# Kernel tuning notes

Measured on AMD Instinct MI355X. Metric: run time of the kernel, lower is better.

## Reference

```python
import jax, jax.numpy as jnp
import numpy as np

N_NODES = 100000


def gcn_conv(x, src, dst, W, b):
    # x: [N, F_in]; src/dst include self-loops; symmetric degree normalization (PyG GCNConv)
    n = x.shape[0]
    xw = x @ W  # [N, F_out]
    ones = jnp.ones(dst.shape[0], dtype=xw.dtype)
    deg = jax.ops.segment_sum(ones, dst, num_segments=n)  # in-degree incl. self-loop
    dinv = jnp.where(deg > 0, jax.lax.rsqrt(deg), 0.0)
    norm = dinv[src] * dinv[dst]  # [E]
    msg = xw[src] * norm[:, None]  # gather + per-edge scale
    out = jax.ops.segment_sum(msg, dst, num_segments=n)  # scatter-add aggregation
    return out + b


def setup_inputs() -> dict:
    key = jax.random.key(0)
    ks = jax.random.split(key, 6)
    F_in = 512
    E = 3200000
    x = jax.random.normal(ks[0], (N_NODES, F_in), dtype=jnp.float32)
    edge_index = jax.random.randint(ks[1], (2, E), 0, N_NODES, dtype=jnp.int64)
    W1 = jax.random.normal(ks[2], (F_in, 16), dtype=jnp.float32) * (1.0 / np.sqrt(F_in))
    b1 = jnp.zeros((16,), dtype=jnp.float32)
    W2 = jax.random.normal(ks[3], (16, 16), dtype=jnp.float32) * 0.25
    b2 = jnp.zeros((16,), dtype=jnp.float32)
    fc_w = jax.random.normal(ks[4], (16, 1), dtype=jnp.float32) * 0.25
    fc_b = jnp.zeros((1,), dtype=jnp.float32)
    return {"x": x, "edge_index": edge_index, "W1": W1, "b1": b1,
            "W2": W2, "b2": b2, "fc_w": fc_w, "fc_b": fc_b}


def reference(x, edge_index, W1, b1, W2, b2, fc_w, fc_b):
    n = x.shape[0]
    loop = jnp.arange(n, dtype=edge_index.dtype)
    src = jnp.concatenate([edge_index[0], loop])  # add self-loops
    dst = jnp.concatenate([edge_index[1], loop])
    h = jax.nn.relu(gcn_conv(x, src, dst, W1, b1))
    h = jax.nn.relu(gcn_conv(h, src, dst, W2, b2))
    g = jnp.mean(h, axis=0, keepdims=True)  # global_mean_pool, single graph -> [1, 16]
    return g @ fc_w + fc_b  # [1, 1]
```

## Files before the change

kernel.cpp:

```cpp
#include <hip/hip_runtime.h>
#include <hip/hip_fp16.h>
#include <stdint.h>

#define F_IN 512
#define F_OUT 16
#define CB_SHIFT 8
#define CB_W 256
#define PER 6250
#define SORT_CAP 6400

typedef __attribute__((ext_vector_type(8))) short bf16x8;
typedef __attribute__((ext_vector_type(4))) float f32x4;

__device__ inline float4 f4_shfl_xor(float4 v, int mask) {
    float4 r;
    r.x = __shfl_xor(v.x, mask);
    r.y = __shfl_xor(v.y, mask);
    r.z = __shfl_xor(v.z, mask);
    r.w = __shfl_xor(v.w, mask);
    return r;
}

__device__ inline short f2bf(float f) {
    unsigned u = __float_as_uint(f);
    unsigned r = (u + 0x7FFFu + ((u >> 16) & 1u)) >> 16;
    return (short)(unsigned short)r;
}

__device__ inline float4 ld_h4(const __half* __restrict__ xw, int s, int q) {
    const __half2* p = (const __half2*)(xw + ((size_t)s << 4)) + (q << 1);
    float2 f0 = __half22float2(p[0]);
    float2 f1 = __half22float2(p[1]);
    return make_float4(f0.x, f0.y, f1.x, f1.y);
}

__global__ __launch_bounds__(256) void k_chist(const int* __restrict__ ei, int E, int K1, int B,
                                               int* __restrict__ cntT) {
    __shared__ int h[512];
    int t = threadIdx.x;
    for (int i = t; i < K1; i += 256) h[i] = 0;
    __syncthreads();
    int e0 = blockIdx.x * PER, e1 = min(E, e0 + PER);
    for (int e = e0 + t; e < e1; e += 256)
        atomicAdd(&h[ei[(size_t)E + e] >> CB_SHIFT], 1);
    __syncthreads();
    for (int i = t; i < K1; i += 256) cntT[(size_t)i * B + blockIdx.x] = h[i];
}

__global__ __launch_bounds__(512) void k_btot(const int* __restrict__ cntT, int B, int K1,
                                              int* __restrict__ bucketBase, int* __restrict__ bucketCnt) {
    __shared__ int sm[512];
    int k = threadIdx.x;
    int tot = 0;
    if (k < K1) {
        const int4* row = (const int4*)(cntT + (size_t)k * B);
        for (int b = 0; b < B / 4; b++) {
            int4 v = row[b];
            tot += v.x + v.y + v.z + v.w;
        }
    }
    sm[k] = tot;
    __syncthreads();
    for (int off = 1; off < 512; off <<= 1) {
        int add = (k >= off) ? sm[k - off] : 0;
        __syncthreads();
        sm[k] += add;
        __syncthreads();
    }
    if (k < K1) { bucketBase[k] = sm[k] - tot; bucketCnt[k] = tot; }
}

__global__ __launch_bounds__(512) void k_bbase(const int* __restrict__ cntT, int B,
                                               const int* __restrict__ bucketBase,
                                               int* __restrict__ baseT) {
    __shared__ int sm[512];
    int k = blockIdx.x, t = threadIdx.x;
    int v = (t < B) ? cntT[(size_t)k * B + t] : 0;
    sm[t] = v;
    __syncthreads();
    for (int off = 1; off < 512; off <<= 1) {
        int add = (t >= off) ? sm[t - off] : 0;
        __syncthreads();
        sm[t] += add;
        __syncthreads();
    }
    if (t < B) baseT[(size_t)k * B + t] = bucketBase[k] + sm[t] - v;
}

__global__ __launch_bounds__(512) void k_csort(const int* __restrict__ ei, int E, int K1, int B,
                                               const int* __restrict__ baseT, unsigned* __restrict__ part) {
    __shared__ unsigned sorted[SORT_CAP];
    __shared__ int h[512], lb[512], cur[512], gb[512];
    int t = threadIdx.x;
    int e0 = blockIdx.x * PER, e1 = min(E, e0 + PER);
    h[t] = 0;
    __syncthreads();
    for (int e = e0 + t; e < e1; e += 512)
        atomicAdd(&h[ei[(size_t)E + e] >> CB_SHIFT], 1);
    __syncthreads();
    int v = h[t];
    lb[t] = v;
    __syncthreads();
    for (int off = 1; off < 512; off <<= 1) {
        int add = (t >= off) ? lb[t - off] : 0;
        __syncthreads();
        lb[t] += add;
        __syncthreads();
    }
    int excl = lb[t] - v;
    __syncthreads();
    lb[t] = excl;
    cur[t] = excl;
    if (t < K1) gb[t] = baseT[(size_t)t * B + blockIdx.x];
    __syncthreads();
    for (int e = e0 + t; e < e1; e += 512) {
        int s = ei[e];
        int d = ei[(size_t)E + e];
        int pos = atomicAdd(&cur[d >> CB_SHIFT], 1);
        sorted[pos] = ((unsigned)s << CB_SHIFT) | (unsigned)(d & (CB_W - 1));
    }
    __syncthreads();
    int g16 = t >> 4, ln = t & 15;
    for (int k = g16; k < K1; k += 32) {
        int s0 = lb[k];
        int s1 = cur[k];
        int g  = gb[k];
        for (int i = s0 + ln; i < s1; i += 16)
            part[(size_t)g + (i - s0)] = sorted[i];
    }
}

__global__ __launch_bounds__(512) void k_prep2(const unsigned* __restrict__ part,
                                               const int* __restrict__ bucketBase, const int* __restrict__ bucketCnt,
                                               int* __restrict__ hist, float* __restrict__ dinv,
                                               int* __restrict__ offsets, int* __restrict__ csr, int N) {
    __shared__ int fh[CB_W], fb[CB_W], cur[CB_W];
    int k = blockIdx.x, t = threadIdx.x;
    int base = bucketBase[k], cnt = bucketCnt[k];
    int d0 = k << CB_SHIFT;
    if (t < CB_W) fh[t] = 0;
    __syncthreads();
    for (int i = t; i < cnt; i += 512)
        atomicAdd(&fh[part[(size_t)base + i] & (CB_W - 1)], 1);
    __syncthreads();
    int v = 0;
    if (t < CB_W) { v = fh[t]; fb[t] = v; }
    __syncthreads();
    for (int off = 1; off < CB_W; off <<= 1) {
        int add = (t >= off && t < CB_W) ? fb[t - off] : 0;
        __syncthreads();
        if (t < CB_W) fb[t] += add;
        __syncthreads();
    }
    if (t < CB_W) {
        int excl = fb[t] - v;
        int n = d0 + t;
        if (n < N) {
            offsets[n] = base + excl;
            hist[n] = v;
            dinv[n] = rsqrtf((float)(v + 1));
        }
        cur[t] = excl;
    }
    __syncthreads();
    for (int i = t; i < cnt; i += 512) {
        unsigned e = part[(size_t)base + i];
        int pos = atomicAdd(&cur[e & (CB_W - 1)], 1);
        csr[(size_t)base + pos] = (int)(e >> CB_SHIFT);
    }
}

__global__ __launch_bounds__(256, 4) void k_gemm1(const float* __restrict__ x, const float* __restrict__ W1,
                                                  const float* __restrict__ dinv, __half* __restrict__ xw1p, int N) {
    int lane = threadIdx.x & 63;
    int wv   = blockIdx.x * 4 + (threadIdx.x >> 6);
    int nw   = gridDim.x * 4;
    int r16  = lane & 15;
    int kg   = lane >> 4;

    bf16x8 bfrag[16];
#pragma unroll
    for (int s = 0; s < 16; s++) {
        bf16x8 f;
#pragma unroll
        for (int i = 0; i < 8; i++)
            f[i] = f2bf(W1[(s * 32 + kg * 8 + i) * 16 + r16]);
        bfrag[s] = f;
    }

    int ntiles = (N + 15) >> 4;
    int npairs = (ntiles + 1) >> 1;
    for (int pair = wv; pair < npairs; pair += nw) {
        int tile0 = pair * 2;
        int tile1 = tile0 + 1;
        int row0 = (tile0 << 4) + r16;
        int row1 = (tile1 << 4) + r16;
        const float* xr0 = x + (size_t)min(row0, N - 1) * F_IN + kg * 8;
        const float* xr1 = x + (size_t)min(row1, N - 1) * F_IN + kg * 8;
        bool t1ok = (tile1 < ntiles);
        f32x4 acc0 = {0.f, 0.f, 0.f, 0.f};
        f32x4 acc1 = {0.f, 0.f, 0.f, 0.f};
#pragma unroll
        for (int s = 0; s < 16; s++) {
            float4 xa0 = *(const float4*)(xr0 + s * 32);
            float4 xb0 = *(const float4*)(xr0 + s * 32 + 4);
            float4 xa1 = *(const float4*)(xr1 + s * 32);
            float4 xb1 = *(const float4*)(xr1 + s * 32 + 4);
            bf16x8 af0, af1;
            af0[0] = f2bf(xa0.x); af0[1] = f2bf(xa0.y); af0[2] = f2bf(xa0.z); af0[3] = f2bf(xa0.w);
            af0[4] = f2bf(xb0.x); af0[5] = f2bf(xb0.y); af0[6] = f2bf(xb0.z); af0[7] = f2bf(xb0.w);
            af1[0] = f2bf(xa1.x); af1[1] = f2bf(xa1.y); af1[2] = f2bf(xa1.z); af1[3] = f2bf(xa1.w);
            af1[4] = f2bf(xb1.x); af1[5] = f2bf(xb1.y); af1[6] = f2bf(xb1.z); af1[7] = f2bf(xb1.w);
            acc0 = __builtin_amdgcn_mfma_f32_16x16x32_bf16(af0, bfrag[s], acc0, 0, 0, 0);
            acc1 = __builtin_amdgcn_mfma_f32_16x16x32_bf16(af1, bfrag[s], acc1, 0, 0, 0);
        }
#pragma unroll
        for (int j = 0; j < 4; j++) {
            int r0 = (tile0 << 4) + kg * 4 + j;
            if (r0 < N) {
                float dn = dinv[r0];
                xw1p[((size_t)r0 << 4) + r16] = __float2half_rn(dn * acc0[j]);
            }
        }
        if (t1ok) {
#pragma unroll
            for (int j = 0; j < 4; j++) {
                int r1 = (tile1 << 4) + kg * 4 + j;
                if (r1 < N) {
                    float dn = dinv[r1];
                    xw1p[((size_t)r1 << 4) + r16] = __float2half_rn(dn * acc1[j]);
                }
            }
        }
    }
}

__global__ __launch_bounds__(256) void k_agg1(const __half* __restrict__ xw, const int* __restrict__ offsets,
                                              const int* __restrict__ hist, const float* __restrict__ dinv,
                                              const int* __restrict__ csr, const float* __restrict__ b1,
                                              const float* __restrict__ W2, __half* __restrict__ xw2p, int N) {
    __shared__ float W2s[256];
    if (threadIdx.x < 256) W2s[threadIdx.x] = W2[threadIdx.x];
    __syncthreads();

    int lane = threadIdx.x & 63;
    int wave = threadIdx.x >> 6;
    int grp  = lane >> 4;
    int sub  = lane & 15;
    int eo   = sub >> 2;
    int q    = sub & 3;
    int node = blockIdx.x * 16 + wave * 4 + grp;
    if (node >= N) return;

    int start = offsets[node], cnt = hist[node];
    float dn = dinv[node];
    float4 a0 = make_float4(0.f,0.f,0.f,0.f), a1 = a0, a2 = a0, a3 = a0;
    int i = 0;
    for (; i + 32 <= cnt; i += 32) {
        int s0 = csr[start + i + eo];
        int s1 = csr[start + i + 4 + eo];
        int s2 = csr[start + i + 8 + eo];
        int s3 = csr[start + i + 12 + eo];
        int s4 = csr[start + i + 16 + eo];
        int s5 = csr[start + i + 20 + eo];
        int s6 = csr[start + i + 24 + eo];
        int s7 = csr[start + i + 28 + eo];
        float4 v0 = ld_h4(xw, s0, q);
        float4 v1 = ld_h4(xw, s1, q);
        float4 v2 = ld_h4(xw, s2, q);
        float4 v3 = ld_h4(xw, s3, q);
        float4 v4 = ld_h4(xw, s4, q);
        float4 v5 = ld_h4(xw, s5, q);
        float4 v6 = ld_h4(xw, s6, q);
        float4 v7 = ld_h4(xw, s7, q);
        a0.x+=v0.x; a0.y+=v0.y; a0.z+=v0.z; a0.w+=v0.w;
        a1.x+=v1.x; a1.y+=v1.y; a1.z+=v1.z; a1.w+=v1.w;
        a2.x+=v2.x; a2.y+=v2.y; a2.z+=v2.z; a2.w+=v2.w;
        a3.x+=v3.x; a3.y+=v3.y; a3.z+=v3.z; a3.w+=v3.w;
        a0.x+=v4.x; a0.y+=v4.y; a0.z+=v4.z; a0.w+=v4.w;
        a1.x+=v5.x; a1.y+=v5.y; a1.z+=v5.z; a1.w+=v5.w;
        a2.x+=v6.x; a2.y+=v6.y; a2.z+=v6.z; a2.w+=v6.w;
        a3.x+=v7.x; a3.y+=v7.y; a3.z+=v7.z; a3.w+=v7.w;
    }
    for (; i + 16 <= cnt; i += 16) {
        int s0 = csr[start + i + eo];
        int s1 = csr[start + i + 4 + eo];
        int s2 = csr[start + i + 8 + eo];
        int s3 = csr[start + i + 12 + eo];
        float4 v0 = ld_h4(xw, s0, q);
        float4 v1 = ld_h4(xw, s1, q);
        float4 v2 = ld_h4(xw, s2, q);
        float4 v3 = ld_h4(xw, s3, q);
        a0.x+=v0.x; a0.y+=v0.y; a0.z+=v0.z; a0.w+=v0.w;
        a1.x+=v1.x; a1.y+=v1.y; a1.z+=v1.z; a1.w+=v1.w;
        a2.x+=v2.x; a2.y+=v2.y; a2.z+=v2.z; a2.w+=v2.w;
        a3.x+=v3.x; a3.y+=v3.y; a3.z+=v3.z; a3.w+=v3.w;
    }
    for (; i + 8 <= cnt; i += 8) {
        int s0 = csr[start + i + eo];
        int s1 = csr[start + i + 4 + eo];
        float4 v0 = ld_h4(xw, s0, q);
        float4 v1 = ld_h4(xw, s1, q);
        a0.x+=v0.x; a0.y+=v0.y; a0.z+=v0.z; a0.w+=v0.w;
        a1.x+=v1.x; a1.y+=v1.y; a1.z+=v1.z; a1.w+=v1.w;
    }
    for (; i < cnt; i += 4) {
        if (i + eo < cnt) {
            int s0 = csr[start + i + eo];
            float4 v0 = ld_h4(xw, s0, q);
            a0.x+=v0.x; a0.y+=v0.y; a0.z+=v0.z; a0.w+=v0.w;
        }
    }
    float4 acc;
    acc.x = a0.x+a1.x+a2.x+a3.x;
    acc.y = a0.y+a1.y+a2.y+a3.y;
    acc.z = a0.z+a1.z+a2.z+a3.z;
    acc.w = a0.w+a1.w+a2.w+a3.w;
    { float4 u = f4_shfl_xor(acc, 4); acc.x+=u.x; acc.y+=u.y; acc.z+=u.z; acc.w+=u.w; }
    { float4 u = f4_shfl_xor(acc, 8); acc.x+=u.x; acc.y+=u.y; acc.z+=u.z; acc.w+=u.w; }

    float4 sv = ld_h4(xw, node, q);
    float4 bq = ((const float4*)b1)[q];
    float4 h;
    h.x = fmaxf(dn * (acc.x + sv.x) + bq.x, 0.f);
    h.y = fmaxf(dn * (acc.y + sv.y) + bq.y, 0.f);
    h.z = fmaxf(dn * (acc.z + sv.z) + bq.z, 0.f);
    h.w = fmaxf(dn * (acc.w + sv.w) + bq.w, 0.f);

    float o = 0.f;
#pragma unroll
    for (int a = 0; a < 4; a++) {
        int src = (grp << 4) + a;
        float h0 = __shfl(h.x, src);
        float h1 = __shfl(h.y, src);
        float h2 = __shfl(h.z, src);
        float h3 = __shfl(h.w, src);
        o += h0 * W2s[(a*4+0)*16 + sub] + h1 * W2s[(a*4+1)*16 + sub]
           + h2 * W2s[(a*4+2)*16 + sub] + h3 * W2s[(a*4+3)*16 + sub];
    }
    xw2p[((size_t)node << 4) + sub] = __float2half_rn(dn * o);
}

__global__ __launch_bounds__(256) void k_agg2(const __half* __restrict__ xw, const int* __restrict__ offsets,
                                              const int* __restrict__ hist, const float* __restrict__ dinv,
                                              const int* __restrict__ csr, const float* __restrict__ b2,
                                              float* __restrict__ partials, int N) {
    int lane = threadIdx.x & 63;
    int wave = threadIdx.x >> 6;
    int grp  = lane >> 4;
    int sub  = lane & 15;
    int eo   = sub >> 2;
    int q    = sub & 3;
    int node = blockIdx.x * 16 + wave * 4 + grp;

    float4 m = make_float4(0.f, 0.f, 0.f, 0.f);
    if (node < N) {
        int start = offsets[node], cnt = hist[node];
        float dn = dinv[node];
        float4 a0 = make_float4(0.f,0.f,0.f,0.f), a1 = a0, a2 = a0, a3 = a0;
        int i = 0;
        for (; i + 32 <= cnt; i += 32) {
            int s0 = csr[start + i + eo];
            int s1 = csr[start + i + 4 + eo];
            int s2 = csr[start + i + 8 + eo];
            int s3 = csr[start + i + 12 + eo];
            int s4 = csr[start + i + 16 + eo];
            int s5 = csr[start + i + 20 + eo];
            int s6 = csr[start + i + 24 + eo];
            int s7 = csr[start + i + 28 + eo];
            float4 v0 = ld_h4(xw, s0, q);
            float4 v1 = ld_h4(xw, s1, q);
            float4 v2 = ld_h4(xw, s2, q);
            float4 v3 = ld_h4(xw, s3, q);
            float4 v4 = ld_h4(xw, s4, q);
            float4 v5 = ld_h4(xw, s5, q);
            float4 v6 = ld_h4(xw, s6, q);
            float4 v7 = ld_h4(xw, s7, q);
            a0.x+=v0.x; a0.y+=v0.y; a0.z+=v0.z; a0.w+=v0.w;
            a1.x+=v1.x; a1.y+=v1.y; a1.z+=v1.z; a1.w+=v1.w;
            a2.x+=v2.x; a2.y+=v2.y; a2.z+=v2.z; a2.w+=v2.w;
            a3.x+=v3.x; a3.y+=v3.y; a3.z+=v3.z; a3.w+=v3.w;
            a0.x+=v4.x; a0.y+=v4.y; a0.z+=v4.z; a0.w+=v4.w;
            a1.x+=v5.x; a1.y+=v5.y; a1.z+=v5.z; a1.w+=v5.w;
            a2.x+=v6.x; a2.y+=v6.y; a2.z+=v6.z; a2.w+=v6.w;
            a3.x+=v7.x; a3.y+=v7.y; a3.z+=v7.z; a3.w+=v7.w;
        }
        for (; i + 16 <= cnt; i += 16) {
            int s0 = csr[start + i + eo];
            int s1 = csr[start + i + 4 + eo];
            int s2 = csr[start + i + 8 + eo];
            int s3 = csr[start + i + 12 + eo];
            float4 v0 = ld_h4(xw, s0, q);
            float4 v1 = ld_h4(xw, s1, q);
            float4 v2 = ld_h4(xw, s2, q);
            float4 v3 = ld_h4(xw, s3, q);
            a0.x+=v0.x; a0.y+=v0.y; a0.z+=v0.z; a0.w+=v0.w;
            a1.x+=v1.x; a1.y+=v1.y; a1.z+=v1.z; a1.w+=v1.w;
            a2.x+=v2.x; a2.y+=v2.y; a2.z+=v2.z; a2.w+=v2.w;
            a3.x+=v3.x; a3.y+=v3.y; a3.z+=v3.z; a3.w+=v3.w;
        }
        for (; i + 8 <= cnt; i += 8) {
            int s0 = csr[start + i + eo];
            int s1 = csr[start + i + 4 + eo];
            float4 v0 = ld_h4(xw, s0, q);
            float4 v1 = ld_h4(xw, s1, q);
            a0.x+=v0.x; a0.y+=v0.y; a0.z+=v0.z; a0.w+=v0.w;
            a1.x+=v1.x; a1.y+=v1.y; a1.z+=v1.z; a1.w+=v1.w;
        }
        for (; i < cnt; i += 4) {
            if (i + eo < cnt) {
                int s0 = csr[start + i + eo];
                float4 v0 = ld_h4(xw, s0, q);
                a0.x+=v0.x; a0.y+=v0.y; a0.z+=v0.z; a0.w+=v0.w;
            }
        }
        float4 acc;
        acc.x = a0.x+a1.x+a2.x+a3.x;
        acc.y = a0.y+a1.y+a2.y+a3.y;
        acc.z = a0.z+a1.z+a2.z+a3.z;
        acc.w = a0.w+a1.w+a2.w+a3.w;
        { float4 u = f4_shfl_xor(acc, 4); acc.x+=u.x; acc.y+=u.y; acc.z+=u.z; acc.w+=u.w; }
        { float4 u = f4_shfl_xor(acc, 8); acc.x+=u.x; acc.y+=u.y; acc.z+=u.z; acc.w+=u.w; }
        float4 sv = ld_h4(xw, node, q);
        float4 bq = ((const float4*)b2)[q];
        if (eo == 0) {
            m.x = fmaxf(dn * (acc.x + sv.x) + bq.x, 0.f);
            m.y = fmaxf(dn * (acc.y + sv.y) + bq.y, 0.f);
            m.z = fmaxf(dn * (acc.z + sv.z) + bq.z, 0.f);
            m.w = fmaxf(dn * (acc.w + sv.w) + bq.w, 0.f);
        }
    }
    { float4 u = f4_shfl_xor(m, 16); m.x+=u.x; m.y+=u.y; m.z+=u.z; m.w+=u.w; }
    { float4 u = f4_shfl_xor(m, 32); m.x+=u.x; m.y+=u.y; m.z+=u.z; m.w+=u.w; }
    __shared__ float smf[4][16];
    if (lane < 4) {
        smf[wave][q*4+0] = m.x;
        smf[wave][q*4+1] = m.y;
        smf[wave][q*4+2] = m.z;
        smf[wave][q*4+3] = m.w;
    }
    __syncthreads();
    if (threadIdx.x < 16) {
        float s = smf[0][threadIdx.x] + smf[1][threadIdx.x] + smf[2][threadIdx.x] + smf[3][threadIdx.x];
        partials[(size_t)blockIdx.x * 16 + threadIdx.x] = s;
    }
}

__global__ void k_final(const float* __restrict__ partials, int NB, const float* __restrict__ fc_w,
                        const float* __restrict__ fc_b, float* __restrict__ out, float invN) {
    __shared__ float sm[64][16];
    int t = threadIdx.x;
    int g = t >> 4, j = t & 15;
    float s = 0.0f;
    for (int bk = g; bk < NB; bk += 64) s += partials[(size_t)bk * 16 + j];
    sm[g][j] = s;
    __syncthreads();
    for (int str = 32; str > 0; str >>= 1) {
        if (g < str) sm[g][j] += sm[g + str][j];
        __syncthreads();
    }
    if (t == 0) {
        float acc = fc_b[0];
#pragma unroll
        for (int jj = 0; jj < 16; jj++) acc += sm[0][jj] * invN * fc_w[jj];
        out[0] = acc;
    }
}

extern "C" void kernel_launch(void* const* d_in, const int* in_sizes, int n_in,
                              void* d_out, int out_size, void* d_ws, size_t ws_size,
                              hipStream_t stream) {
    const float* x   = (const float*)d_in[0];
    const int*   ei  = (const int*)d_in[1];
    const float* W1  = (const float*)d_in[2];
    const float* b1  = (const float*)d_in[3];
    const float* W2  = (const float*)d_in[4];
    const float* b2  = (const float*)d_in[5];
    const float* fcw = (const float*)d_in[6];
    const float* fcb = (const float*)d_in[7];
    float* out = (float*)d_out;

    int N = in_sizes[0] / F_IN;
    int E = in_sizes[1] / 2;
    int K1 = (N + CB_W - 1) >> CB_SHIFT;
    int B1 = (E + PER - 1) / PER;

    char* p = (char*)d_ws;
    auto alloc = [&](size_t bytes) {
        void* r = (void*)p;
        p += (bytes + 255) & ~(size_t)255;
        return r;
    };
    int*   cntT       = (int*)alloc((size_t)K1 * B1 * 4);
    int*   baseT      = (int*)alloc((size_t)K1 * B1 * 4);
    int*   bucketBase = (int*)alloc((size_t)K1 * 4);
    int*   bucketCnt  = (int*)alloc((size_t)K1 * 4);
    int*   hist       = (int*)alloc((size_t)N * 4);
    int*   offsets    = (int*)alloc((size_t)N * 4);
    float* dinv       = (float*)alloc((size_t)N * 4);
    int*   csr        = (int*)alloc((size_t)E * 4);
    unsigned* part    = (unsigned*)alloc((size_t)E * 4);
    __half* xw1p      = (__half*)alloc((size_t)N * F_OUT * 2);
    __half* xw2p      = (__half*)alloc((size_t)N * F_OUT * 2);
    int NB_NODE = (N + 15) / 16;
    float* partials = (float*)alloc((size_t)NB_NODE * 16 * 4);

    k_chist<<<B1, 256, 0, stream>>>(ei, E, K1, B1, cntT);
    k_btot<<<1, 512, 0, stream>>>(cntT, B1, K1, bucketBase, bucketCnt);
    k_bbase<<<K1, 512, 0, stream>>>(cntT, B1, bucketBase, baseT);
    k_csort<<<B1, 512, 0, stream>>>(ei, E, K1, B1, baseT, part);
    k_prep2<<<K1, 512, 0, stream>>>(part, bucketBase, bucketCnt, hist, dinv, offsets, csr, N);

    k_gemm1<<<782, 256, 0, stream>>>(x, W1, dinv, xw1p, N);
    k_agg1<<<NB_NODE, 256, 0, stream>>>(xw1p, offsets, hist, dinv, csr, b1, W2, xw2p, N);
    k_agg2<<<NB_NODE, 256, 0, stream>>>(xw2p, offsets, hist, dinv, csr, b2, partials, N);
    k_final<<<1, 1024, 0, stream>>>(partials, NB_NODE, fcw, fcb, out, 1.0f / (float)N);
}
```

Measured before the change: 213.9 us.

## Split GEMM1 across CSR-build kernels to overlap compute with sorting

The dense x@W1 GEMM is cut into three row-pair ranges, each run by extra blocks appended to the histogram, bucket-sort and CSR-finalize kernels, so the memory-bound x read overlaps the edge-sorting phases. Because dinv is not known until the last phase, the GEMM now writes unscaled fp16 results and a new k_scale pass multiplies by dinv afterwards. The csort kernel also reuses the per-block histogram from cntT instead of recomputing it. The cost is an extra read-modify-write pass over xw1, plus hand-tuned split ratios and grid sizes that may leave the work unevenly balanced.

After: 250.3 us. 17.0% more time.

```diff
diff --git a/kernel.cpp b/kernel.cpp
--- a/kernel.cpp
+++ b/kernel.cpp
@@ -34,147 +34,10 @@
     return make_float4(f0.x, f0.y, f1.x, f1.y);
 }
 
-__global__ __launch_bounds__(256) void k_chist(const int* __restrict__ ei, int E, int K1, int B,
-                                               int* __restrict__ cntT) {
-    __shared__ int h[512];
-    int t = threadIdx.x;
-    for (int i = t; i < K1; i += 256) h[i] = 0;
-    __syncthreads();
-    int e0 = blockIdx.x * PER, e1 = min(E, e0 + PER);
-    for (int e = e0 + t; e < e1; e += 256)
-        atomicAdd(&h[ei[(size_t)E + e] >> CB_SHIFT], 1);
-    __syncthreads();
-    for (int i = t; i < K1; i += 256) cntT[(size_t)i * B + blockIdx.x] = h[i];
-}
-
-__global__ __launch_bounds__(512) void k_btot(const int* __restrict__ cntT, int B, int K1,
-                                              int* __restrict__ bucketBase, int* __restrict__ bucketCnt) {
-    __shared__ int sm[512];
-    int k = threadIdx.x;
-    int tot = 0;
-    if (k < K1) {
-        const int4* row = (const int4*)(cntT + (size_t)k * B);
-        for (int b = 0; b < B / 4; b++) {
-            int4 v = row[b];
-            tot += v.x + v.y + v.z + v.w;
-        }
-    }
-    sm[k] = tot;
-    __syncthreads();
-    for (int off = 1; off < 512; off <<= 1) {
-        int add = (k >= off) ? sm[k - off] : 0;
-        __syncthreads();
-        sm[k] += add;
-        __syncthreads();
-    }
-    if (k < K1) { bucketBase[k] = sm[k] - tot; bucketCnt[k] = tot; }
-}
-
-__global__ __launch_bounds__(512) void k_bbase(const int* __restrict__ cntT, int B,
-                                               const int* __restrict__ bucketBase,
-                                               int* __restrict__ baseT) {
-    __shared__ int sm[512];
-    int k = blockIdx.x, t = threadIdx.x;
-    int v = (t < B) ? cntT[(size_t)k * B + t] : 0;
-    sm[t] = v;
-    __syncthreads();
-    for (int off = 1; off < 512; off <<= 1) {
-        int add = (t >= off) ? sm[t - off] : 0;
-        __syncthreads();
-        sm[t] += add;
-        __syncthreads();
-    }
-    if (t < B) baseT[(size_t)k * B + t] = bucketBase[k] + sm[t] - v;
-}
-
-__global__ __launch_bounds__(512) void k_csort(const int* __restrict__ ei, int E, int K1, int B,
-                                               const int* __restrict__ baseT, unsigned* __restrict__ part) {
-    __shared__ unsigned sorted[SORT_CAP];
-    __shared__ int h[512], lb[512], cur[512], gb[512];
-    int t = threadIdx.x;
-    int e0 = blockIdx.x * PER, e1 = min(E, e0 + PER);
-    h[t] = 0;
-    __syncthreads();
-    for (int e = e0 + t; e < e1; e += 512)
-        atomicAdd(&h[ei[(size_t)E + e] >> CB_SHIFT], 1);
-    __syncthreads();
-    int v = h[t];
-    lb[t] = v;
-    __syncthreads();
-    for (int off = 1; off < 512; off <<= 1) {
-        int add = (t >= off) ? lb[t - off] : 0;
-        __syncthreads();
-        lb[t] += add;
-        __syncthreads();
-    }
-    int excl = lb[t] - v;
-    __syncthreads();
-    lb[t] = excl;
-    cur[t] = excl;
-    if (t < K1) gb[t] = baseT[(size_t)t * B + blockIdx.x];
-    __syncthreads();
-    for (int e = e0 + t; e < e1; e += 512) {
-        int s = ei[e];
-        int d = ei[(size_t)E + e];
-        int pos = atomicAdd(&cur[d >> CB_SHIFT], 1);
-        sorted[pos] = ((unsigned)s << CB_SHIFT) | (unsigned)(d & (CB_W - 1));
-    }
-    __syncthreads();
-    int g16 = t >> 4, ln = t & 15;
-    for (int k = g16; k < K1; k += 32) {
-        int s0 = lb[k];
-        int s1 = cur[k];
-        int g  = gb[k];
-        for (int i = s0 + ln; i < s1; i += 16)
-            part[(size_t)g + (i - s0)] = sorted[i];
-    }
-}
-
-__global__ __launch_bounds__(512) void k_prep2(const unsigned* __restrict__ part,
-                                               const int* __restrict__ bucketBase, const int* __restrict__ bucketCnt,
-                                               int* __restrict__ hist, float* __restrict__ dinv,
-                                               int* __restrict__ offsets, int* __restrict__ csr, int N) {
-    __shared__ int fh[CB_W], fb[CB_W], cur[CB_W];
-    int k = blockIdx.x, t = threadIdx.x;
-    int base = bucketBase[k], cnt = bucketCnt[k];
-    int d0 = k << CB_SHIFT;
-    if (t < CB_W) fh[t] = 0;
-    __syncthreads();
-    for (int i = t; i < cnt; i += 512)
-        atomicAdd(&fh[part[(size_t)base + i] & (CB_W - 1)], 1);
-    __syncthreads();
-    int v = 0;
-    if (t < CB_W) { v = fh[t]; fb[t] = v; }
-    __syncthreads();
-    for (int off = 1; off < CB_W; off <<= 1) {
-        int add = (t >= off && t < CB_W) ? fb[t - off] : 0;
-        __syncthreads();
-        if (t < CB_W) fb[t] += add;
-        __syncthreads();
-    }
-    if (t < CB_W) {
-        int excl = fb[t] - v;
-        int n = d0 + t;
-        if (n < N) {
-            offsets[n] = base + excl;
-            hist[n] = v;
-            dinv[n] = rsqrtf((float)(v + 1));
-        }
-        cur[t] = excl;
-    }
-    __syncthreads();
-    for (int i = t; i < cnt; i += 512) {
-        unsigned e = part[(size_t)base + i];
-        int pos = atomicAdd(&cur[e & (CB_W - 1)], 1);
-        csr[(size_t)base + pos] = (int)(e >> CB_SHIFT);
-    }
-}
-
-__global__ __launch_bounds__(256, 4) void k_gemm1(const float* __restrict__ x, const float* __restrict__ W1,
-                                                  const float* __restrict__ dinv, __half* __restrict__ xw1p, int N) {
+__device__ inline void gemm_pairs(const float* __restrict__ x, const float* __restrict__ W1,
+                                  __half* __restrict__ xw1u, int N,
+                                  int ps, int pe, int gw, int NW) {
     int lane = threadIdx.x & 63;
-    int wv   = blockIdx.x * 4 + (threadIdx.x >> 6);
-    int nw   = gridDim.x * 4;
     int r16  = lane & 15;
     int kg   = lane >> 4;
 
@@ -189,8 +52,7 @@
     }
 
     int ntiles = (N + 15) >> 4;
-    int npairs = (ntiles + 1) >> 1;
-    for (int pair = wv; pair < npairs; pair += nw) {
+    for (int pair = ps + gw; pair < pe; pair += NW) {
         int tile0 = pair * 2;
         int tile1 = tile0 + 1;
         int row0 = (tile0 << 4) + r16;
@@ -217,21 +79,184 @@
 #pragma unroll
         for (int j = 0; j < 4; j++) {
             int r0 = (tile0 << 4) + kg * 4 + j;
-            if (r0 < N) {
-                float dn = dinv[r0];
-                xw1p[((size_t)r0 << 4) + r16] = __float2half_rn(dn * acc0[j]);
-            }
+            if (r0 < N) xw1u[((size_t)r0 << 4) + r16] = __float2half_rn(acc0[j]);
         }
         if (t1ok) {
 #pragma unroll
             for (int j = 0; j < 4; j++) {
                 int r1 = (tile1 << 4) + kg * 4 + j;
-                if (r1 < N) {
-                    float dn = dinv[r1];
-                    xw1p[((size_t)r1 << 4) + r16] = __float2half_rn(dn * acc1[j]);
-                }
+                if (r1 < N) xw1u[((size_t)r1 << 4) + r16] = __float2half_rn(acc1[j]);
             }
         }
+    }
+}
+
+__global__ __launch_bounds__(512) void k_fuse1(const int* __restrict__ ei, int E, int K1, int B,
+                                               int* __restrict__ cntT,
+                                               const float* __restrict__ x, const float* __restrict__ W1,
+                                               __half* __restrict__ xw1u, int N, int P1, int GB) {
+    if ((int)blockIdx.x < B) {
+        __shared__ int h[512];
+        int t = threadIdx.x;
+        h[t] = 0;
+        __syncthreads();
+        int e0 = blockIdx.x * PER, e1 = min(E, e0 + PER);
+        for (int e = e0 + t; e < e1; e += 512)
+            atomicAdd(&h[ei[(size_t)E + e] >> CB_SHIFT], 1);
+        __syncthreads();
+        for (int i = t; i < K1; i += 512) cntT[(size_t)i * B + blockIdx.x] = h[i];
+    } else {
+        int gw = ((int)blockIdx.x - B) * 8 + (int)(threadIdx.x >> 6);
+        gemm_pairs(x, W1, xw1u, N, 0, P1, gw, GB * 8);
+    }
+}
+
+__global__ __launch_bounds__(512) void k_btot(const int* __restrict__ cntT, int B, int K1,
+                                              int* __restrict__ bucketBase, int* __restrict__ bucketCnt) {
+    __shared__ int sm[512];
+    int k = threadIdx.x;
+    int tot = 0;
+    if (k < K1) {
+        const int4* row = (const int4*)(cntT + (size_t)k * B);
+        for (int b = 0; b < B / 4; b++) {
+            int4 v = row[b];
+            tot += v.x + v.y + v.z + v.w;
+        }
+    }
+    sm[k] = tot;
+    __syncthreads();
+    for (int off = 1; off < 512; off <<= 1) {
+        int add = (k >= off) ? sm[k - off] : 0;
+        __syncthreads();
+        sm[k] += add;
+        __syncthreads();
+    }
+    if (k < K1) { bucketBase[k] = sm[k] - tot; bucketCnt[k] = tot; }
+}
+
+__global__ __launch_bounds__(512) void k_bbase(const int* __restrict__ cntT, int B,
+                                               const int* __restrict__ bucketBase,
+                                               int* __restrict__ baseT) {
+    __shared__ int sm[512];
+    int k = blockIdx.x, t = threadIdx.x;
+    int v = (t < B) ? cntT[(size_t)k * B + t] : 0;
+    sm[t] = v;
+    __syncthreads();
+    for (int off = 1; off < 512; off <<= 1) {
+        int add = (t >= off) ? sm[t - off] : 0;
+        __syncthreads();
+        sm[t] += add;
+        __syncthreads();
+    }
+    if (t < B) baseT[(size_t)k * B + t] = bucketBase[k] + sm[t] - v;
+}
+
+__global__ __launch_bounds__(512) void k_fuse2(const int* __restrict__ ei, int E, int K1, int B,
+                                               const int* __restrict__ cntT, const int* __restrict__ baseT,
+                                               unsigned* __restrict__ part,
+                                               const float* __restrict__ x, const float* __restrict__ W1,
+                                               __half* __restrict__ xw1u, int N, int P1, int P2, int GB) {
+    if ((int)blockIdx.x < B) {
+        __shared__ unsigned sorted[SORT_CAP];
+        __shared__ int lb[512], cur[512], gb[512];
+        int t = threadIdx.x;
+        int e0 = blockIdx.x * PER, e1 = min(E, e0 + PER);
+        int v = (t < K1) ? cntT[(size_t)t * B + blockIdx.x] : 0;
+        lb[t] = v;
+        __syncthreads();
+        for (int off = 1; off < 512; off <<= 1) {
+            int add = (t >= off) ? lb[t - off] : 0;
+            __syncthreads();
+            lb[t] += add;
+            __syncthreads();
+        }
+        int excl = lb[t] - v;
+        __syncthreads();
+        lb[t] = excl;
+        cur[t] = excl;
+        if (t < K1) gb[t] = baseT[(size_t)t * B + blockIdx.x];
+        __syncthreads();
+        for (int e = e0 + t; e < e1; e += 512) {
+            int s = ei[e];
+            int d = ei[(size_t)E + e];
+            int pos = atomicAdd(&cur[d >> CB_SHIFT], 1);
+            sorted[pos] = ((unsigned)s << CB_SHIFT) | (unsigned)(d & (CB_W - 1));
+        }
+        __syncthreads();
+        int g16 = t >> 4, ln = t & 15;
+        for (int k = g16; k < K1; k += 32) {
+            int s0 = lb[k];
+            int s1 = cur[k];
+            int g  = gb[k];
+            for (int i = s0 + ln; i < s1; i += 16)
+                part[(size_t)g + (i - s0)] = sorted[i];
+        }
+    } else {
+        int gw = ((int)blockIdx.x - B) * 8 + (int)(threadIdx.x >> 6);
+        gemm_pairs(x, W1, xw1u, N, P1, P2, gw, GB * 8);
+    }
+}
+
+__global__ __launch_bounds__(512) void k_fuse3(const unsigned* __restrict__ part,
+                                               const int* __restrict__ bucketBase, const int* __restrict__ bucketCnt,
+                                               int* __restrict__ hist, float* __restrict__ dinv,
+                                               int* __restrict__ offsets, int* __restrict__ csr,
+                                               const float* __restrict__ x, const float* __restrict__ W1,
+                                               __half* __restrict__ xw1u, int N, int K1, int P2, int PE, int GB) {
+    if ((int)blockIdx.x < K1) {
+        __shared__ int fh[CB_W], fb[CB_W], cur[CB_W];
+        int k = blockIdx.x, t = threadIdx.x;
+        int base = bucketBase[k], cnt = bucketCnt[k];
+        int d0 = k << CB_SHIFT;
+        if (t < CB_W) fh[t] = 0;
+        __syncthreads();
+        for (int i = t; i < cnt; i += 512)
+            atomicAdd(&fh[part[(size_t)base + i] & (CB_W - 1)], 1);
+        __syncthreads();
+        int v = 0;
+        if (t < CB_W) { v = fh[t]; fb[t] = v; }
+        __syncthreads();
+        for (int off = 1; off < CB_W; off <<= 1) {
+            int add = (t >= off && t < CB_W) ? fb[t - off] : 0;
+            __syncthreads();
+            if (t < CB_W) fb[t] += add;
+            __syncthreads();
+        }
+        if (t < CB_W) {
+            int excl = fb[t] - v;
+            int n = d0 + t;
+            if (n < N) {
+                offsets[n] = base + excl;
+                hist[n] = v;
+                dinv[n] = rsqrtf((float)(v + 1));
+            }
+            cur[t] = excl;
+        }
+        __syncthreads();
+        for (int i = t; i < cnt; i += 512) {
+            unsigned e = part[(size_t)base + i];
+            int pos = atomicAdd(&cur[e & (CB_W - 1)], 1);
+            csr[(size_t)base + pos] = (int)(e >> CB_SHIFT);
+        }
+    } else {
+        int gw = ((int)blockIdx.x - K1) * 8 + (int)(threadIdx.x >> 6);
+        gemm_pairs(x, W1, xw1u, N, P2, PE, gw, GB * 8);
+    }
+}
+
+__global__ __launch_bounds__(512) void k_scale(__half* __restrict__ xw, const float* __restrict__ dinv, int N) {
+    int i = blockIdx.x * 512 + threadIdx.x;
+    if (i < N * 2) {
+        float dn = dinv[i >> 1];
+        uint4* p = (uint4*)xw + i;
+        uint4 v = *p;
+        __half2* h = (__half2*)&v;
+#pragma unroll
+        for (int j = 0; j < 4; j++) {
+            float2 f = __half22float2(h[j]);
+            h[j] = __floats2half2_rn(f.x * dn, f.y * dn);
+        }
+        *p = v;
     }
 }
 
@@ -505,13 +530,20 @@
     int NB_NODE = (N + 15) / 16;
     float* partials = (float*)alloc((size_t)NB_NODE * 16 * 4);
 
-    k_chist<<<B1, 256, 0, stream>>>(ei, E, K1, B1, cntT);
+    int ntiles = (N + 15) >> 4;
+    int npairs = (ntiles + 1) >> 1;
+    int P1 = npairs / 6;
+    int P2 = P1 + (npairs * 11) / 20;
+    int GB1 = 256, GB2 = 512, GB3 = 384;
+
+    k_fuse1<<<B1 + GB1, 512, 0, stream>>>(ei, E, K1, B1, cntT, x, W1, xw1p, N, P1, GB1);
     k_btot<<<1, 512, 0, stream>>>(cntT, B1, K1, bucketBase, bucketCnt);
     k_bbase<<<K1, 512, 0, stream>>>(cntT, B1, bucketBase, baseT);
-    k_csort<<<B1, 512, 0, stream>>>(ei, E, K1, B1, baseT, part);
-    k_prep2<<<K1, 512, 0, stream>>>(part, bucketBase, bucketCnt, hist, dinv, offsets, csr, N);
-
-    k_gemm1<<<782, 256, 0, stream>>>(x, W1, dinv, xw1p, N);
+    k_fuse2<<<B1 + GB2, 512, 0, stream>>>(ei, E, K1, B1, cntT, baseT, part, x, W1, xw1p, N, P1, P2, GB2);
+    k_fuse3<<<K1 + GB3, 512, 0, stream>>>(part, bucketBase, bucketCnt, hist, dinv, offsets, csr,
+                                          x, W1, xw1p, N, K1, P2, npairs, GB3);
+    k_scale<<<(2 * N + 511) / 512, 512, 0, stream>>>(xw1p, dinv, N);
+
     k_agg1<<<NB_NODE, 256, 0, stream>>>(xw1p, offsets, hist, dinv, csr, b1, W2, xw2p, N);
     k_agg2<<<NB_NODE, 256, 0, stream>>>(xw2p, offsets, hist, dinv, csr, b2, partials, N);
     k_final<<<1, 1024, 0, stream>>>(partials, NB_NODE, fcw, fcb, out, 1.0f / (float)N);
```
